# Optimization experiments

Measured on AMD Instinct MI355X. Metric: run time of the kernel, lower is better.

## Reference

```python
import jax, jax.numpy as jnp
import numpy as np

N_NODES = 10000
N_EDGES = 320000
IN_CH = 128
HID = 64
HEADS = 8
OUT_CH = 2
NEG_SLOPE = 0.2  # PyG GATConv default
EPS = 1e-16      # PyG softmax denominator eps


def setup_inputs() -> dict:
    key = jax.random.key(0)
    ks = jax.random.split(key, 12)
    x = jax.random.normal(ks[0], (N_NODES, IN_CH), dtype=jnp.float32)
    edge_index = jax.random.randint(ks[1], (2, N_EDGES), 0, N_NODES, dtype=jnp.int64)
    s = 0.05
    W1 = jax.random.normal(ks[2], (IN_CH, HEADS * HID), dtype=jnp.float32) * s
    a_src1 = jax.random.normal(ks[3], (HEADS, HID), dtype=jnp.float32) * s
    a_dst1 = jax.random.normal(ks[4], (HEADS, HID), dtype=jnp.float32) * s
    b1 = jnp.zeros((HEADS * HID,), dtype=jnp.float32)
    W2 = jax.random.normal(ks[5], (HEADS * HID, HID), dtype=jnp.float32) * s
    a_src2 = jax.random.normal(ks[6], (1, HID), dtype=jnp.float32) * s
    a_dst2 = jax.random.normal(ks[7], (1, HID), dtype=jnp.float32) * s
    b2 = jnp.zeros((HID,), dtype=jnp.float32)
    Wc = jax.random.normal(ks[8], (HID, OUT_CH), dtype=jnp.float32) * s
    bc = jnp.zeros((OUT_CH,), dtype=jnp.float32)
    return dict(x=x, edge_index=edge_index, W1=W1, a_src1=a_src1, a_dst1=a_dst1,
                b1=b1, W2=W2, a_src2=a_src2, a_dst2=a_dst2, b2=b2, Wc=Wc, bc=bc)


def gat_layer(x, src, dst, W, a_src, a_dst, bias, heads, ch, concat):
    # x: [N, F_in]; src/dst: [E] (self-loops already appended)
    N = x.shape[0]
    h = (x @ W).reshape(N, heads, ch)                 # [N, H, C]
    e_src = jnp.einsum('nhc,hc->nh', h, a_src)        # [N, H]
    e_dst = jnp.einsum('nhc,hc->nh', h, a_dst)
    e = jax.nn.leaky_relu(e_src[src] + e_dst[dst], NEG_SLOPE)  # [E, H]
    # segment softmax over destination nodes (max-shift has zero gradient)
    m = jax.lax.stop_gradient(jax.ops.segment_max(e, dst, num_segments=N))
    w = jnp.exp(e - m[dst])
    denom = jax.ops.segment_sum(w, dst, num_segments=N)
    alpha = w / (denom[dst] + EPS)                    # [E, H]
    # scatter-aggregate weighted source features
    out = jax.ops.segment_sum(h[src] * alpha[:, :, None], dst, num_segments=N)  # [N,H,C]
    out = out.reshape(N, heads * ch) if concat else out.mean(axis=1)
    return out + bias


def reference(x, edge_index, W1, a_src1, a_dst1, b1, W2, a_src2, a_dst2, b2, Wc, bc):
    N = x.shape[0]
    loop = jnp.arange(N, dtype=edge_index.dtype)
    src = jnp.concatenate([edge_index[0], loop])  # PyG add_self_loops=True
    dst = jnp.concatenate([edge_index[1], loop])
    h1 = gat_layer(x, src, dst, W1, a_src1, a_dst1, b1, HEADS, HID, True)
    h1 = jax.nn.elu(h1)
    # dropout is identity in eval mode
    h2 = gat_layer(h1, src, dst, W2, a_src2, a_dst2, b2, 1, HID, False)
    return h2 @ Wc + bc  # [N, 2]
```

## Files before the change

kernel.cpp:

```cpp
#include <hip/hip_runtime.h>
#include <hip/hip_bf16.h>

#define N_NODES 10000
#define N_EDGES 320000
#define IN_CH 128
#define HID 64
#define HEADS 8
#define OUT_CH 2
#define BM 64
#define BK 16
#define ZERO_BLOCKS 16
#define BCAP 128

__device__ __forceinline__ unsigned short f2bf(float f) {
    union { float f; unsigned u; } v; v.f = f;
    unsigned r = (v.u + 0x7FFFu + ((v.u >> 16) & 1u)) >> 16;
    return (unsigned short)r;
}

__global__ __launch_bounds__(256) void gemm1_and_zero(
    const float* __restrict__ A,
    const float* __restrict__ W1,
    const float* __restrict__ a_src1,
    const float* __restrict__ a_dst1,
    unsigned short* __restrict__ hfeatP,
    float* __restrict__ esAll,
    float* __restrict__ edAll,
    int* __restrict__ cursor,
    int M) {
    __shared__ float As[BK][BM + 4];
    __shared__ float Bs[BK][64 + 4];
    int bx = blockIdx.x;
    int tid = threadIdx.x;

    if (bx < ZERO_BLOCKS) {
        for (int i = bx * 256 + tid; i < N_NODES; i += ZERO_BLOCKS * 256)
            cursor[i] = 0;
        return;
    }

    int vb = bx - ZERO_BLOCKS;
    int h  = vb & 7;
    int bm = (vb >> 3) * BM;
    const float* B = W1 + h * 64;
    int tx = tid & 15, ty = tid >> 4;
    int ar = tid >> 2, ac = (tid & 3) * 4;
    int agr = bm + ar;
    int br = tid >> 4, bc = (tid & 15) * 4;
    float4 av, bv;
    av = (agr < M) ? *(const float4*)&A[(size_t)agr * IN_CH + ac]
                   : make_float4(0.f, 0.f, 0.f, 0.f);
    bv = *(const float4*)&B[(size_t)br * (HEADS * HID) + bc];
    float acc[4][4] = {};
    for (int k0 = 0; k0 < IN_CH; k0 += BK) {
        As[ac + 0][ar] = av.x; As[ac + 1][ar] = av.y;
        As[ac + 2][ar] = av.z; As[ac + 3][ar] = av.w;
        *(float4*)&Bs[br][bc] = bv;
        __syncthreads();
        if (k0 + BK < IN_CH) {
            av = (agr < M)
                ? *(const float4*)&A[(size_t)agr * IN_CH + (k0 + BK) + ac]
                : make_float4(0.f, 0.f, 0.f, 0.f);
            bv = *(const float4*)&B[(size_t)(k0 + BK + br) * (HEADS * HID) + bc];
        }
        #pragma unroll
        for (int k = 0; k < BK; k++) {
            float4 a4 = *(const float4*)&As[k][ty * 4];
            float4 b4 = *(const float4*)&Bs[k][tx * 4];
            float a[4] = {a4.x, a4.y, a4.z, a4.w};
            float b[4] = {b4.x, b4.y, b4.z, b4.w};
            #pragma unroll
            for (int i = 0; i < 4; i++)
                #pragma unroll
                for (int j = 0; j < 4; j++) acc[i][j] += a[i] * b[j];
        }
        __syncthreads();
    }
    float asv[4], adv[4];
    #pragma unroll
    for (int j = 0; j < 4; j++) {
        asv[j] = a_src1[h * 64 + tx * 4 + j];
        adv[j] = a_dst1[h * 64 + tx * 4 + j];
    }
    int ph = h >> 1, hs = h & 1;
    #pragma unroll
    for (int i = 0; i < 4; i++) {
        int gr = bm + ty * 4 + i;
        if (gr >= M) continue;
        float sp = 0.f, dp = 0.f;
        ushort4 pk;
        pk.x = f2bf(acc[i][0]); pk.y = f2bf(acc[i][1]);
        pk.z = f2bf(acc[i][2]); pk.w = f2bf(acc[i][3]);
        *(ushort4*)&hfeatP[((size_t)ph * M + gr) * 128 + hs * 64 + tx * 4] = pk;
        #pragma unroll
        for (int j = 0; j < 4; j++) {
            sp += acc[i][j] * asv[j];
            dp += acc[i][j] * adv[j];
        }
        #pragma unroll
        for (int off = 1; off < 16; off <<= 1) {
            sp += __shfl_xor(sp, off, 64);
            dp += __shfl_xor(dp, off, 64);
        }
        if (tx == 0) {
            esAll[(size_t)h * M + gr] = sp;
            edAll[(size_t)h * M + gr] = dp;
        }
    }
}

__global__ void fill_bucket(const int* __restrict__ src,
                            const int* __restrict__ dst, int E,
                            int* cursor, int* __restrict__ bucket) {
    int i = blockIdx.x * blockDim.x + threadIdx.x;
    if (i < E) {
        int d = dst[i];
        int pos = atomicAdd(&cursor[d], 1);
        bucket[(d << 7) + min(pos, BCAP - 1)] = src[i];
    }
}

__global__ __launch_bounds__(256) void gemm2_splitk(
    const float* __restrict__ h1,
    const float* __restrict__ W2,
    float* __restrict__ partial,
    int M) {
    __shared__ float As[BK][BM + 4];
    __shared__ float Bs[BK][64 + 4];
    int tid = threadIdx.x;
    int bm = blockIdx.x * BM;
    int h  = blockIdx.y;
    const float* B = W2 + (size_t)h * 64 * 64;
    float* C = partial + (size_t)h * M * 64;
    int tx = tid & 15, ty = tid >> 4;
    float acc[4][4] = {};
    for (int k0 = 0; k0 < 64; k0 += BK) {
        #pragma unroll
        for (int i = 0; i < 4; i++) {
            int e = tid + i * 256;
            int r = e >> 4, c = e & 15;
            int gr = bm + r;
            As[c][r] = (gr < M)
                ? h1[(size_t)gr * 512 + h * 64 + k0 + c] : 0.f;
        }
        #pragma unroll
        for (int i = 0; i < 4; i++) {
            int e = tid + i * 256;
            int r = e >> 6, c = e & 63;
            Bs[r][c] = B[(size_t)(k0 + r) * 64 + c];
        }
        __syncthreads();
        #pragma unroll
        for (int k = 0; k < BK; k++) {
            float4 a4 = *(const float4*)&As[k][ty * 4];
            float4 b4 = *(const float4*)&Bs[k][tx * 4];
            float a[4] = {a4.x, a4.y, a4.z, a4.w};
            float b[4] = {b4.x, b4.y, b4.z, b4.w};
            #pragma unroll
            for (int i = 0; i < 4; i++)
                #pragma unroll
                for (int j = 0; j < 4; j++) acc[i][j] += a[i] * b[j];
        }
        __syncthreads();
    }
    #pragma unroll
    for (int i = 0; i < 4; i++) {
        int gr = bm + ty * 4 + i;
        if (gr >= M) continue;
        #pragma unroll
        for (int j = 0; j < 4; j++)
            C[(size_t)gr * 64 + tx * 4 + j] = acc[i][j];
    }
}

__global__ __launch_bounds__(256) void gemm2_reduce(
    const float* __restrict__ partial,
    const float* __restrict__ a_src2, const float* __restrict__ a_dst2,
    float* __restrict__ hfeat2, float* __restrict__ es2, float* __restrict__ ed2,
    int M) {
    int n = blockIdx.x * 4 + (threadIdx.x >> 6);
    int l = threadIdx.x & 63;
    if (n >= M) return;
    float v = 0.f;
    #pragma unroll
    for (int h = 0; h < 8; h++)
        v += partial[(size_t)h * M * 64 + (size_t)n * 64 + l];
    hfeat2[(size_t)n * 64 + l] = v;
    float s = v * a_src2[l], t = v * a_dst2[l];
    #pragma unroll
    for (int off = 32; off; off >>= 1) {
        s += __shfl_down(s, off, 64);
        t += __shfl_down(t, off, 64);
    }
    if (l == 0) { es2[n] = s; ed2[n] = t; }
}

__global__ __launch_bounds__(256) void gat_agg_pair(
    const unsigned short* __restrict__ hfeatP, const float* __restrict__ esAll,
    const float* __restrict__ edAll, const int* __restrict__ bucket,
    const int* __restrict__ cursor, const float* __restrict__ b1,
    float* __restrict__ h1, int M) {
    int bx = blockIdx.x;
    int p = bx & 3;
    int n = (bx >> 2) * 4 + (threadIdx.x >> 6);
    int l = threadIdx.x & 63;
    int g = l >> 4;
    int q = l & 15;
    int hq = q >> 3;
    int sub = l & 31;
    int hs = l >> 5;
    int g4 = g << 2;
    int hbaseB = hq << 7;
    const char* hptr = (const char*)hfeatP + (size_t)p * M * 256 + (q << 4);
    const float* esS = esAll + (size_t)(p * 2 + hs) * M;
    float ednS = edAll[(size_t)(p * 2 + hs) * M + n];
    int start = n << 7;
    int deg = min(cursor[n], 96);
    int total = deg + 1;

    float a[8] = {};
    float dloc = 0.f;
    for (int base = 0; base < total; base += 32) {
        int idx = base + sub;
        int sld = bucket[start + idx];
        int sv = (idx < deg) ? sld : n;
        float wgt = 0.f;
        if (idx <= deg) {
            float e = esS[sv] + ednS;
            e = (e > 0.f) ? e : 0.2f * e;
            wgt = __expf(e);
        }
        dloc += wgt;
        int rb = sv << 8;
        int wb = __float_as_int(wgt);
        int cnt = min(32, total - base);
        for (int i = 0; i < cnt; i += 4) {
            int b0 = (i << 2) + g4;
            int rbg = __builtin_amdgcn_ds_bpermute(b0, rb);
            float wg = __int_as_float(
                __builtin_amdgcn_ds_bpermute(b0 + hbaseB, wb));
            const uint4 hv = *(const uint4*)(hptr + rbg);
            a[0] += wg * __uint_as_float(hv.x << 16);
            a[1] += wg * __uint_as_float(hv.x & 0xFFFF0000u);
            a[2] += wg * __uint_as_float(hv.y << 16);
            a[3] += wg * __uint_as_float(hv.y & 0xFFFF0000u);
            a[4] += wg * __uint_as_float(hv.z << 16);
            a[5] += wg * __uint_as_float(hv.z & 0xFFFF0000u);
            a[6] += wg * __uint_as_float(hv.w << 16);
            a[7] += wg * __uint_as_float(hv.w & 0xFFFF0000u);
        }
    }
    #pragma unroll
    for (int off = 16; off; off >>= 1) dloc += __shfl_xor(dloc, off, 64);
    float dother = __shfl_xor(dloc, 32, 64);
    #pragma unroll
    for (int k = 0; k < 8; k++) {
        a[k] += __shfl_xor(a[k], 16, 64);
        a[k] += __shfl_xor(a[k], 32, 64);
    }
    if (g == 0) {
        float d = (hq == 0) ? dloc : dother;
        d += 1e-16f;
        float inv = __builtin_amdgcn_rcpf(d);
        inv = inv * __fmaf_rn(-d, inv, 2.0f);
        const float4 b0v = *(const float4*)&b1[p * 128 + q * 8];
        const float4 b4v = *(const float4*)&b1[p * 128 + q * 8 + 4];
        float vv[8];
        vv[0] = a[0] * inv + b0v.x; vv[1] = a[1] * inv + b0v.y;
        vv[2] = a[2] * inv + b0v.z; vv[3] = a[3] * inv + b0v.w;
        vv[4] = a[4] * inv + b4v.x; vv[5] = a[5] * inv + b4v.y;
        vv[6] = a[6] * inv + b4v.z; vv[7] = a[7] * inv + b4v.w;
        #pragma unroll
        for (int k = 0; k < 8; k++)
            vv[k] = (vv[k] > 0.f) ? vv[k] : (__expf(vv[k]) - 1.f);
        float* dst = &h1[(size_t)n * 512 + p * 128 + q * 8];
        *(float4*)dst = make_float4(vv[0], vv[1], vv[2], vv[3]);
        *(float4*)(dst + 4) = make_float4(vv[4], vv[5], vv[6], vv[7]);
    }
}

__global__ __launch_bounds__(256) void gat_agg2(
    const float* __restrict__ hfeat2, const float* __restrict__ es,
    const float* __restrict__ ed, const int* __restrict__ bucket,
    const int* __restrict__ cursor, const float* __restrict__ b2,
    const float* __restrict__ Wc, const float* __restrict__ bc,
    float* __restrict__ out) {
    int n = blockIdx.x * 4 + (threadIdx.x >> 6);
    int l = threadIdx.x & 63;
    int g = l >> 4;
    int q = l & 15;
    int g4 = g << 2;
    int qoff = q << 4;
    int start = n << 7;
    int deg = min(cursor[n], 96);
    int total = deg + 1;
    float edn = ed[n];

    float ax = 0.f, ay = 0.f, az = 0.f, aw = 0.f;
    float dloc = 0.f;
    for (int base = 0; base < total; base += 64) {
        int cnt = min(64, total - base);
        float wgt = 0.f;
        int sv = n;
        if (l < cnt) {
            int idx = base + l;
            sv = (idx < deg) ? bucket[start + idx] : n;
            float e = es[sv] + edn;
            e = (e > 0.f) ? e : 0.2f * e;
            wgt = __expf(e);
        }
        dloc += wgt;
        int rb = sv << 8;
        int wb = __float_as_int(wgt);
        for (int i = 0; i < cnt; i += 4) {
            int bidx = (i << 2) + g4;
            int rbg = __builtin_amdgcn_ds_bpermute(bidx, rb);
            float wg = __int_as_float(__builtin_amdgcn_ds_bpermute(bidx, wb));
            const float4 hv = *(const float4*)((const char*)hfeat2 + (rbg + qoff));
            ax += wg * hv.x;
            ay += wg * hv.y;
            az += wg * hv.z;
            aw += wg * hv.w;
        }
    }
    float d = dloc;
    #pragma unroll
    for (int off = 32; off; off >>= 1) d += __shfl_down(d, off, 64);
    d = __shfl(d, 0, 64) + 1e-16f;
    float inv = __builtin_amdgcn_rcpf(d);
    inv = inv * __fmaf_rn(-d, inv, 2.0f);
    ax += __shfl_down(ax, 32, 64); ay += __shfl_down(ay, 32, 64);
    az += __shfl_down(az, 32, 64); aw += __shfl_down(aw, 32, 64);
    ax += __shfl_down(ax, 16, 64); ay += __shfl_down(ay, 16, 64);
    az += __shfl_down(az, 16, 64); aw += __shfl_down(aw, 16, 64);
    float p0 = 0.f, p1 = 0.f;
    if (g == 0) {
        const float4 bq = *(const float4*)&b2[q * 4];
        float h0 = ax * inv + bq.x, h1v = ay * inv + bq.y;
        float h2v = az * inv + bq.z, h3 = aw * inv + bq.w;
        const float2* WcV = (const float2*)Wc;
        float2 w0 = WcV[q * 4 + 0], w1 = WcV[q * 4 + 1];
        float2 w2 = WcV[q * 4 + 2], w3 = WcV[q * 4 + 3];
        p0 = h0 * w0.x + h1v * w1.x + h2v * w2.x + h3 * w3.x;
        p1 = h0 * w0.y + h1v * w1.y + h2v * w2.y + h3 * w3.y;
    }
    #pragma unroll
    for (int off = 1; off < 16; off <<= 1) {
        p0 += __shfl_xor(p0, off, 64);
        p1 += __shfl_xor(p1, off, 64);
    }
    if (l == 0) {
        out[n * 2 + 0] = p0 + bc[0];
        out[n * 2 + 1] = p1 + bc[1];
    }
}

extern "C" void kernel_launch(void* const* d_in, const int* in_sizes, int n_in,
                              void* d_out, int out_size, void* d_ws, size_t ws_size,
                              hipStream_t stream) {
    const float* x      = (const float*)d_in[0];
    const int*   eidx   = (const int*)d_in[1];
    const float* W1     = (const float*)d_in[2];
    const float* a_src1 = (const float*)d_in[3];
    const float* a_dst1 = (const float*)d_in[4];
    const float* b1     = (const float*)d_in[5];
    const float* W2     = (const float*)d_in[6];
    const float* a_src2 = (const float*)d_in[7];
    const float* a_dst2 = (const float*)d_in[8];
    const float* b2     = (const float*)d_in[9];
    const float* Wc     = (const float*)d_in[10];
    const float* bc     = (const float*)d_in[11];
    float* out = (float*)d_out;

    const int N = N_NODES, E = N_EDGES;
    const int* esrc = eidx;
    const int* edst = eidx + E;

    size_t off = 0;
    auto alloc = [&](size_t bytes) {
        void* p = (char*)d_ws + off;
        off += (bytes + 255) & ~(size_t)255;
        return p;
    };
    int*   cursor   = (int*)alloc((size_t)N * 4);
    int*   bucket   = (int*)alloc((size_t)N * BCAP * 4);
    unsigned short* hfeatP = (unsigned short*)alloc((size_t)4 * N * 128 * 2);
    float* h1       = (float*)alloc((size_t)N * 512 * 4);
    float* partial  = (float*)alloc((size_t)HEADS * N * 64 * 4);
    float* hfeat2   = (float*)alloc((size_t)N * 64 * 4);
    float* esAll    = (float*)alloc((size_t)HEADS * N * 4);
    float* edAll    = (float*)alloc((size_t)HEADS * N * 4);
    float* es2      = (float*)alloc((size_t)N * 4);
    float* ed2      = (float*)alloc((size_t)N * 4);

    gemm1_and_zero<<<ZERO_BLOCKS + 157 * 8, 256, 0, stream>>>(
        x, W1, a_src1, a_dst1, hfeatP, esAll, edAll, cursor, N);
    fill_bucket<<<(E + 255) / 256, 256, 0, stream>>>(esrc, edst, E, cursor, bucket);
    gat_agg_pair<<<(N / 4) * 4, 256, 0, stream>>>(hfeatP, esAll, edAll,
                                                  bucket, cursor, b1, h1, N);
    dim3 gg2((N + BM - 1) / BM, HEADS);
    gemm2_splitk<<<gg2, 256, 0, stream>>>(h1, W2, partial, N);
    gemm2_reduce<<<(N + 3) / 4, 256, 0, stream>>>(partial, a_src2, a_dst2,
                                                  hfeat2, es2, ed2, N);
    gat_agg2<<<(N + 3) / 4, 256, 0, stream>>>(hfeat2, es2, ed2, bucket, cursor,
                                              b2, Wc, bc, out);
}
```

Before: 193.4 us.

## Replace FP32 GEMM1 with split-bf16 MFMA kernel and a preprocessing split pass

```diff
diff --git a/kernel.cpp b/kernel.cpp
--- a/kernel.cpp
+++ b/kernel.cpp
@@ -9,8 +9,11 @@
 #define OUT_CH 2
 #define BM 64
 #define BK 16
-#define ZERO_BLOCKS 16
 #define BCAP 128
+#define MPAD 10048
+
+typedef __attribute__((ext_vector_type(8))) short frag8;
+typedef __attribute__((ext_vector_type(4))) float f32x4;
 
 __device__ __forceinline__ unsigned short f2bf(float f) {
     union { float f; unsigned u; } v; v.f = f;
@@ -18,94 +21,169 @@
     return (unsigned short)r;
 }
 
-__global__ __launch_bounds__(256) void gemm1_and_zero(
-    const float* __restrict__ A,
-    const float* __restrict__ W1,
-    const float* __restrict__ a_src1,
-    const float* __restrict__ a_dst1,
+__device__ __forceinline__ void g2l16(const void* g, void* l) {
+    __builtin_amdgcn_global_load_lds(
+        (__attribute__((address_space(1))) unsigned int*)g,
+        (__attribute__((address_space(3))) unsigned int*)l, 16, 0, 0);
+}
+
+__global__ __launch_bounds__(256) void prep_split(
+    const float* __restrict__ x, const float* __restrict__ W1,
+    unsigned short* __restrict__ xh, unsigned short* __restrict__ xl,
+    unsigned short* __restrict__ w1h, unsigned short* __restrict__ w1l,
+    int* __restrict__ cursor) {
+    int bx = blockIdx.x, tid = threadIdx.x;
+    if (bx < 628) {
+        int idx = bx * 256 + tid;
+        int row = idx >> 4, c = idx & 15;
+        float f[8];
+        if (row < N_NODES) {
+            float4 v0 = *(const float4*)&x[(size_t)row * IN_CH + c * 8];
+            float4 v1 = *(const float4*)&x[(size_t)row * IN_CH + c * 8 + 4];
+            f[0] = v0.x; f[1] = v0.y; f[2] = v0.z; f[3] = v0.w;
+            f[4] = v1.x; f[5] = v1.y; f[6] = v1.z; f[7] = v1.w;
+        } else {
+            #pragma unroll
+            for (int j = 0; j < 8; j++) f[j] = 0.f;
+        }
+        unsigned short hb[8], lb[8];
+        #pragma unroll
+        for (int j = 0; j < 8; j++) {
+            hb[j] = f2bf(f[j]);
+            float hf = __uint_as_float((unsigned)hb[j] << 16);
+            lb[j] = f2bf(f[j] - hf);
+        }
+        size_t o = ((size_t)row * 16 + (c ^ (row & 15))) * 8;
+        *(ushort4*)&xh[o]     = make_ushort4(hb[0], hb[1], hb[2], hb[3]);
+        *(ushort4*)&xh[o + 4] = make_ushort4(hb[4], hb[5], hb[6], hb[7]);
+        *(ushort4*)&xl[o]     = make_ushort4(lb[0], lb[1], lb[2], lb[3]);
+        *(ushort4*)&xl[o + 4] = make_ushort4(lb[4], lb[5], lb[6], lb[7]);
+    } else if (bx < 660) {
+        int idx = (bx - 628) * 256 + tid;
+        int kb = idx >> 9, c = idx & 511;
+        int hh = c >> 6, cc = c & 63;
+        unsigned short hb[8], lb[8];
+        #pragma unroll
+        for (int i = 0; i < 8; i++) {
+            float v = W1[(size_t)(kb * 8 + i) * (HEADS * HID) + c];
+            hb[i] = f2bf(v);
+            float hf = __uint_as_float((unsigned)hb[i] << 16);
+            lb[i] = f2bf(v - hf);
+        }
+        size_t o = (((size_t)hh * 16 + kb) * 64 + cc) * 8;
+        *(ushort4*)&w1h[o]     = make_ushort4(hb[0], hb[1], hb[2], hb[3]);
+        *(ushort4*)&w1h[o + 4] = make_ushort4(hb[4], hb[5], hb[6], hb[7]);
+        *(ushort4*)&w1l[o]     = make_ushort4(lb[0], lb[1], lb[2], lb[3]);
+        *(ushort4*)&w1l[o + 4] = make_ushort4(lb[4], lb[5], lb[6], lb[7]);
+    } else {
+        int idx = (bx - 660) * 256 + tid;
+        if (idx < 2500) *(int4*)&cursor[idx * 4] = make_int4(0, 0, 0, 0);
+    }
+}
+
+__global__ __launch_bounds__(256) void gemm1_mfma(
+    const unsigned short* __restrict__ xh, const unsigned short* __restrict__ xl,
+    const unsigned short* __restrict__ w1h, const unsigned short* __restrict__ w1l,
+    const float* __restrict__ a_src1, const float* __restrict__ a_dst1,
     unsigned short* __restrict__ hfeatP,
-    float* __restrict__ esAll,
-    float* __restrict__ edAll,
-    int* __restrict__ cursor,
-    int M) {
-    __shared__ float As[BK][BM + 4];
-    __shared__ float Bs[BK][64 + 4];
-    int bx = blockIdx.x;
+    float* __restrict__ esAll, float* __restrict__ edAll, int M) {
+    __shared__ alignas(16) unsigned short Ah[8192];
+    __shared__ alignas(16) unsigned short Al[8192];
+    __shared__ alignas(16) unsigned short Bh[8192];
+    __shared__ alignas(16) unsigned short Bl[8192];
     int tid = threadIdx.x;
-
-    if (bx < ZERO_BLOCKS) {
-        for (int i = bx * 256 + tid; i < N_NODES; i += ZERO_BLOCKS * 256)
-            cursor[i] = 0;
-        return;
-    }
-
-    int vb = bx - ZERO_BLOCKS;
+    int lane = tid & 63, w = tid >> 6;
+    int vb = (blockIdx.x & 7) * 157 + (blockIdx.x >> 3);
     int h  = vb & 7;
     int bm = (vb >> 3) * BM;
-    const float* B = W1 + h * 64;
-    int tx = tid & 15, ty = tid >> 4;
-    int ar = tid >> 2, ac = (tid & 3) * 4;
-    int agr = bm + ar;
-    int br = tid >> 4, bc = (tid & 15) * 4;
-    float4 av, bv;
-    av = (agr < M) ? *(const float4*)&A[(size_t)agr * IN_CH + ac]
-                   : make_float4(0.f, 0.f, 0.f, 0.f);
-    bv = *(const float4*)&B[(size_t)br * (HEADS * HID) + bc];
-    float acc[4][4] = {};
-    for (int k0 = 0; k0 < IN_CH; k0 += BK) {
-        As[ac + 0][ar] = av.x; As[ac + 1][ar] = av.y;
-        As[ac + 2][ar] = av.z; As[ac + 3][ar] = av.w;
-        *(float4*)&Bs[br][bc] = bv;
-        __syncthreads();
-        if (k0 + BK < IN_CH) {
-            av = (agr < M)
-                ? *(const float4*)&A[(size_t)agr * IN_CH + (k0 + BK) + ac]
-                : make_float4(0.f, 0.f, 0.f, 0.f);
-            bv = *(const float4*)&B[(size_t)(k0 + BK + br) * (HEADS * HID) + bc];
-        }
-        #pragma unroll
-        for (int k = 0; k < BK; k++) {
-            float4 a4 = *(const float4*)&As[k][ty * 4];
-            float4 b4 = *(const float4*)&Bs[k][tx * 4];
-            float a[4] = {a4.x, a4.y, a4.z, a4.w};
-            float b[4] = {b4.x, b4.y, b4.z, b4.w};
-            #pragma unroll
-            for (int i = 0; i < 4; i++)
-                #pragma unroll
-                for (int j = 0; j < 4; j++) acc[i][j] += a[i] * b[j];
-        }
-        __syncthreads();
-    }
+
+    {
+        const unsigned short* gAh = xh  + (size_t)bm * 128;
+        const unsigned short* gAl = xl  + (size_t)bm * 128;
+        const unsigned short* gBh = w1h + (size_t)h * 8192;
+        const unsigned short* gBl = w1l + (size_t)h * 8192;
+        #pragma unroll
+        for (int i = 0; i < 4; i++) {
+            int s = w * 4 + i;
+            int go = s * 512 + lane * 8;
+            g2l16(gAh + go, &Ah[s * 512]);
+            g2l16(gAl + go, &Al[s * 512]);
+            g2l16(gBh + go, &Bh[s * 512]);
+            g2l16(gBl + go, &Bl[s * 512]);
+        }
+    }
+    __syncthreads();
+
+    int col = lane & 15, g4 = lane >> 4;
+    int arow = w * 16 + col;
+    f32x4 acc[4] = {};
+    #pragma unroll
+    for (int ks = 0; ks < 4; ks++) {
+        int ai = (arow * 16 + ((ks * 4 + g4) ^ col)) * 8;
+        frag8 ah = *(const frag8*)&Ah[ai];
+        frag8 al = *(const frag8*)&Al[ai];
+        #pragma unroll
+        for (int ct = 0; ct < 4; ct++) {
+            int bi = ((ks * 4 + g4) * 64 + ct * 16 + col) * 8;
+            frag8 bhv = *(const frag8*)&Bh[bi];
+            frag8 blv = *(const frag8*)&Bl[bi];
+            acc[ct] = __builtin_amdgcn_mfma_f32_16x16x32_bf16(ah, bhv, acc[ct], 0, 0, 0);
+            acc[ct] = __builtin_amdgcn_mfma_f32_16x16x32_bf16(al, bhv, acc[ct], 0, 0, 0);
+            acc[ct] = __builtin_amdgcn_mfma_f32_16x16x32_bf16(ah, blv, acc[ct], 0, 0, 0);
+        }
+    }
+
     float asv[4], adv[4];
     #pragma unroll
-    for (int j = 0; j < 4; j++) {
-        asv[j] = a_src1[h * 64 + tx * 4 + j];
-        adv[j] = a_dst1[h * 64 + tx * 4 + j];
-    }
-    int ph = h >> 1, hs = h & 1;
-    #pragma unroll
-    for (int i = 0; i < 4; i++) {
-        int gr = bm + ty * 4 + i;
-        if (gr >= M) continue;
-        float sp = 0.f, dp = 0.f;
-        ushort4 pk;
-        pk.x = f2bf(acc[i][0]); pk.y = f2bf(acc[i][1]);
-        pk.z = f2bf(acc[i][2]); pk.w = f2bf(acc[i][3]);
-        *(ushort4*)&hfeatP[((size_t)ph * M + gr) * 128 + hs * 64 + tx * 4] = pk;
-        #pragma unroll
-        for (int j = 0; j < 4; j++) {
-            sp += acc[i][j] * asv[j];
-            dp += acc[i][j] * adv[j];
+    for (int ct = 0; ct < 4; ct++) {
+        asv[ct] = a_src1[h * 64 + ct * 16 + col];
+        adv[ct] = a_dst1[h * 64 + ct * 16 + col];
+    }
+    #pragma unroll
+    for (int r = 0; r < 4; r++) {
+        float s = 0.f, d = 0.f;
+        #pragma unroll
+        for (int ct = 0; ct < 4; ct++) {
+            s += acc[ct][r] * asv[ct];
+            d += acc[ct][r] * adv[ct];
         }
         #pragma unroll
         for (int off = 1; off < 16; off <<= 1) {
-            sp += __shfl_xor(sp, off, 64);
-            dp += __shfl_xor(dp, off, 64);
-        }
-        if (tx == 0) {
-            esAll[(size_t)h * M + gr] = sp;
-            edAll[(size_t)h * M + gr] = dp;
-        }
+            s += __shfl_xor(s, off, 64);
+            d += __shfl_xor(d, off, 64);
+        }
+        if (col == 0) {
+            int gr = bm + w * 16 + g4 * 4 + r;
+            if (gr < M) {
+                esAll[(size_t)h * M + gr] = s;
+                edAll[(size_t)h * M + gr] = d;
+            }
+        }
+    }
+
+    __syncthreads();
+    unsigned short* Tr = Ah;
+    int wrow = w * 16 + g4 * 4;
+    #pragma unroll
+    for (int ct = 0; ct < 4; ct++)
+        #pragma unroll
+        for (int r = 0; r < 4; r++)
+            Tr[(wrow + r) * 68 + ct * 16 + col] = f2bf(acc[ct][r]);
+    __syncthreads();
+    int row = tid >> 2, q = tid & 3;
+    int gr = bm + row;
+    if (gr < M) {
+        int tb = row * 68 + q * 16;
+        ushort4 t0 = *(const ushort4*)&Tr[tb];
+        ushort4 t1 = *(const ushort4*)&Tr[tb + 4];
+        ushort4 t2 = *(const ushort4*)&Tr[tb + 8];
+        ushort4 t3 = *(const ushort4*)&Tr[tb + 12];
+        unsigned short* dst =
+            &hfeatP[(((size_t)(h >> 1) * M + gr) * 128) + (h & 1) * 64 + q * 16];
+        *(ushort4*)&dst[0]  = t0;
+        *(ushort4*)&dst[4]  = t1;
+        *(ushort4*)&dst[8]  = t2;
+        *(ushort4*)&dst[12] = t3;
     }
 }
 
@@ -392,9 +470,14 @@
     float* edAll    = (float*)alloc((size_t)HEADS * N * 4);
     float* es2      = (float*)alloc((size_t)N * 4);
     float* ed2      = (float*)alloc((size_t)N * 4);
-
-    gemm1_and_zero<<<ZERO_BLOCKS + 157 * 8, 256, 0, stream>>>(
-        x, W1, a_src1, a_dst1, hfeatP, esAll, edAll, cursor, N);
+    unsigned short* xh  = (unsigned short*)alloc((size_t)MPAD * 128 * 2);
+    unsigned short* xl  = (unsigned short*)alloc((size_t)MPAD * 128 * 2);
+    unsigned short* w1h = (unsigned short*)alloc((size_t)128 * 512 * 2);
+    unsigned short* w1l = (unsigned short*)alloc((size_t)128 * 512 * 2);
+
+    prep_split<<<670, 256, 0, stream>>>(x, W1, xh, xl, w1h, w1l, cursor);
+    gemm1_mfma<<<157 * 8, 256, 0, stream>>>(xh, xl, w1h, w1l, a_src1, a_dst1,
+                                            hfeatP, esAll, edAll, N);
     fill_bucket<<<(E + 255) / 256, 256, 0, stream>>>(esrc, edst, E, cursor, bucket);
     gat_agg_pair<<<(N / 4) * 4, 256, 0, stream>>>(hfeatP, esAll, edAll,
                                                   bucket, cursor, b1, h1, N);
```

New measurement: 183.2 us. 5.3% less time.
